# Kernel optimization log

Hardware: AMD Instinct MI355X
Metric: run time of the kernel (lower is better)

Reference implementation:

```python
import jax, jax.numpy as jnp
import numpy as np

N_GRAPHS = 32
N_NODES = 2048          # nodes per graph == lstm1 input_size
N_TOTAL = N_GRAPHS * N_NODES
N_EDGES = 1048576
HEADS = 8
GAT_OUT = 12            # per-head GAT output dim (== num_features)
OUT_CH = 9
NEG_SLOPE = 0.2
BN_EPS = 1e-5


def setup_inputs() -> dict:
    key = jax.random.key(0)
    ks = jax.random.split(key, 20)
    inp = {}
    inp['x'] = jax.random.normal(ks[0], (N_TOTAL, GAT_OUT), jnp.float32)
    inp['edge_index'] = jax.random.randint(ks[1], (2, N_EDGES), 0, N_TOTAL, jnp.int64)
    inp['W_gat'] = jax.random.normal(ks[2], (GAT_OUT, HEADS * GAT_OUT), jnp.float32) * 0.3
    inp['a_src'] = jax.random.normal(ks[3], (HEADS, GAT_OUT), jnp.float32) * 0.3
    inp['a_dst'] = jax.random.normal(ks[4], (HEADS, GAT_OUT), jnp.float32) * 0.3
    inp['gat_bias'] = jax.random.normal(ks[5], (GAT_OUT,), jnp.float32) * 0.1
    inp['bn_gamma'] = jax.random.uniform(ks[6], (GAT_OUT,), jnp.float32, 0.5, 1.5)
    inp['bn_beta'] = jax.random.normal(ks[7], (GAT_OUT,), jnp.float32) * 0.1
    inp['bn_mean'] = jax.random.normal(ks[8], (GAT_OUT,), jnp.float32) * 0.1
    inp['bn_var'] = jax.random.uniform(ks[9], (GAT_OUT,), jnp.float32, 0.5, 1.5)
    inp['w_ih1'] = jax.random.normal(ks[10], (4 * 32, N_NODES), jnp.float32) / np.sqrt(N_NODES)
    inp['w_hh1'] = jax.random.normal(ks[11], (4 * 32, 32), jnp.float32) / np.sqrt(32)
    inp['b_ih1'] = jnp.zeros((4 * 32,), jnp.float32)
    inp['b_hh1'] = jnp.zeros((4 * 32,), jnp.float32)
    inp['w_ih2'] = jax.random.normal(ks[12], (4 * 128, 32), jnp.float32) / np.sqrt(32)
    inp['w_hh2'] = jax.random.normal(ks[13], (4 * 128, 128), jnp.float32) / np.sqrt(128)
    inp['b_ih2'] = jnp.zeros((4 * 128,), jnp.float32)
    inp['b_hh2'] = jnp.zeros((4 * 128,), jnp.float32)
    inp['lin_w'] = jax.random.normal(ks[14], (N_NODES, 128), jnp.float32) / np.sqrt(128)
    inp['lin_b'] = jax.random.normal(ks[15], (N_NODES,), jnp.float32) * 0.1
    return inp


def _gat(x, edge_index, W, a_src, a_dst, bias):
    # PyG GATConv, heads=HEADS, out=GAT_OUT, concat=False (mean over heads), eval mode.
    N = x.shape[0]
    xp = (x @ W).reshape(N, HEADS, GAT_OUT)               # [N,H,C]
    loops = jnp.arange(N, dtype=edge_index.dtype)
    src = jnp.concatenate([edge_index[0], loops])
    dst = jnp.concatenate([edge_index[1], loops])
    asrc = jnp.einsum('nhc,hc->nh', xp, a_src)            # [N,H]
    adst = jnp.einsum('nhc,hc->nh', xp, a_dst)
    e = jax.nn.leaky_relu(asrc[src] + adst[dst], NEG_SLOPE)  # [E,H]
    m = jax.ops.segment_max(e, dst, num_segments=N)
    e = jnp.exp(e - m[dst])
    denom = jax.ops.segment_sum(e, dst, num_segments=N)
    alpha = e / (denom[dst] + 1e-16)
    msg = xp[src] * alpha[:, :, None]                     # [E,H,C]
    out = jax.ops.segment_sum(msg, dst, num_segments=N)   # [N,H,C]
    return out.mean(axis=1) + bias                        # concat=False -> head mean


def _lstm(x_seq, w_ih, w_hh, b_ih, b_hh):
    # x_seq: [T,B,I]; PyTorch gate order i,f,g,o.
    Hh = w_hh.shape[1]
    B = x_seq.shape[1]
    bias = b_ih + b_hh

    def step(carry, xt):
        h, c = carry
        gates = xt @ w_ih.T + h @ w_hh.T + bias
        i, f, g, o = jnp.split(gates, 4, axis=-1)
        c = jax.nn.sigmoid(f) * c + jax.nn.sigmoid(i) * jnp.tanh(g)
        h = jax.nn.sigmoid(o) * jnp.tanh(c)
        return (h, c), h

    init = (jnp.zeros((B, Hh), x_seq.dtype), jnp.zeros((B, Hh), x_seq.dtype))
    _, hs = jax.lax.scan(step, init, x_seq)
    return hs


def reference(x, edge_index, W_gat, a_src, a_dst, gat_bias,
              bn_gamma, bn_beta, bn_mean, bn_var,
              w_ih1, w_hh1, b_ih1, b_hh1,
              w_ih2, w_hh2, b_ih2, b_hh2,
              lin_w, lin_b):
    h = _gat(x, edge_index, W_gat, a_src, a_dst, gat_bias)          # [N,12]
    h = (h - bn_mean) / jnp.sqrt(bn_var + BN_EPS) * bn_gamma + bn_beta
    # dropout inactive in eval mode
    h = jax.nn.log_softmax(h, axis=1)
    h = h.reshape(N_GRAPHS, N_NODES, GAT_OUT)
    h = jnp.moveaxis(h, 2, 0)                                       # [T=12,B,n]
    h = _lstm(h, w_ih1, w_hh1, b_ih1, b_hh1)                        # [12,B,32]
    h = _lstm(h, w_ih2, w_hh2, b_ih2, b_hh2)                        # [12,B,128]
    h = h @ lin_w.T + lin_b                                         # [12,B,n]
    h = h[-OUT_CH:]                                                 # [9,B,n]
    h = jnp.moveaxis(h, 0, 2)                                       # [B,n,9]
    return h.reshape(N_GRAPHS * N_NODES, OUT_CH)
```

## Files before the change

kernel.cpp:

```cpp
#include <hip/hip_runtime.h>
#include <math.h>

#define N_EDGES_C 1048576
#define N_TOTAL_C 65536

typedef _Float16 h2v __attribute__((ext_vector_type(2)));
typedef int i4v __attribute__((ext_vector_type(4)));

#if defined(__has_builtin)
#if __has_builtin(__builtin_amdgcn_fdot2)
#define HAS_FDOT2 1
#endif
#endif

__device__ __forceinline__ float fdot2(h2v a, h2v b, float c) {
#ifdef HAS_FDOT2
    return __builtin_amdgcn_fdot2(a, b, c, false);
#else
    return c + (float)a.x * (float)b.x + (float)a.y * (float)b.y;
#endif
}

__device__ __forceinline__ float sigf(float x){ return 1.0f/(1.0f+expf(-x)); }
__device__ __forceinline__ float lrelu(float x){ return (x>=0.f)? x : 0.2f*x; }


__global__ void prep_kernel(const float* __restrict__ x, const float* __restrict__ Wg,
                            const float* __restrict__ a_src, const float* __restrict__ a_dst,
                            _Float16* __restrict__ xpp)
{
    int tid = threadIdx.x;
    __shared__ float Ws[12*96];
    __shared__ float as_s[96], ad_s[96];
    for (int i = tid; i < 1152; i += 256) Ws[i] = Wg[i];
    if (tid < 96) { as_s[tid] = a_src[tid]; ad_s[tid] = a_dst[tid]; }
    __syncthreads();
    int gid = blockIdx.x * 256 + tid;
    int n = gid >> 3;
    int h = gid & 7;
    const float4* xv = (const float4*)(x + (size_t)n * 12);
    float4 v0 = xv[0], v1 = xv[1], v2 = xv[2];
    float xr[12] = {v0.x,v0.y,v0.z,v0.w, v1.x,v1.y,v1.z,v1.w, v2.x,v2.y,v2.z,v2.w};
    float xp_[12];
    #pragma unroll
    for (int c = 0; c < 12; c++) {
        float acc = 0.f;
        #pragma unroll
        for (int k = 0; k < 12; k++) acc += xr[k] * Ws[k*96 + h*12 + c];
        xp_[c] = acc;
    }
    float sa = 0.f, sd = 0.f;
    #pragma unroll
    for (int c = 0; c < 12; c++) { sa += xp_[c]*as_s[h*12+c]; sd += xp_[c]*ad_s[h*12+c]; }
    union { _Float16 hh[16]; float ff[8]; float4 f4[2]; } s;
    #pragma unroll
    for (int c = 0; c < 12; c++) s.hh[c] = (_Float16)xp_[c];
    s.ff[6] = sa;
    s.ff[7] = sd;
    float4* o = (float4*)(xpp + (size_t)gid * 16);
    o[0] = s.f4[0];
    o[1] = s.f4[1];
}

__global__ __launch_bounds__(256)
void edge_hist(const int* __restrict__ ei, unsigned* __restrict__ cnt,
               unsigned* __restrict__ rank8)
{
    __shared__ unsigned hist[16384];
    int tid = threadIdx.x;
    int slice = blockIdx.x;
    for (int i = tid; i < 16384; i += 256) hist[i] = 0;
    __syncthreads();
    const i4v* dst4 = (const i4v*)(ei + N_EDGES_C) + slice*2048;
    for (int i = tid; i < 2048; i += 256) {
        i4v d = __builtin_nontemporal_load(&dst4[i]);
        int dd[4] = {d.x, d.y, d.z, d.w};
        unsigned packed = 0;
        #pragma unroll
        for (int j = 0; j < 4; j++) {
            int dj = dd[j];
            unsigned sh = (unsigned)(dj & 3) << 3;
            unsigned old = atomicAdd(&hist[dj >> 2], 1u << sh);
            packed |= ((old >> sh) & 0xffu) << (j*8);
        }
        __builtin_nontemporal_store(packed, &rank8[slice*2048 + i]);
    }
    __syncthreads();
    unsigned* cg = cnt + (size_t)slice*16384;
    for (int i = tid; i < 16384; i += 256) cg[i] = hist[i];
}

__global__ void slice_prefix(unsigned* __restrict__ cnt, int* __restrict__ deg)
{
    int w = blockIdx.x*256 + threadIdx.x;
    unsigned run = 0;
    unsigned* base = cnt + w;
    for (int s = 0; s < 128; s++) {
        unsigned v = base[(size_t)s*16384];
        base[(size_t)s*16384] = run;
        run += v;
    }
    ((int4*)deg)[w] = make_int4((int)(run & 255u), (int)((run >> 8) & 255u),
                                (int)((run >> 16) & 255u), (int)(run >> 24));
}

__global__ void scan_build(const int* __restrict__ deg, int* __restrict__ rowptr)
{
    __shared__ int sums[1024];
    int tid = threadIdx.x;
    int4 v[16];
    const int4* deg4 = (const int4*)deg;
    #pragma unroll
    for (int j = 0; j < 16; j++) v[j] = deg4[tid*16 + j];
    int s = 0;
    #pragma unroll
    for (int j = 0; j < 16; j++) s += v[j].x + v[j].y + v[j].z + v[j].w;
    sums[tid] = s;
    __syncthreads();
    for (int off = 1; off < 1024; off <<= 1) {
        int t = 0;
        if (tid >= off) t = sums[tid - off];
        __syncthreads();
        if (tid >= off) sums[tid] += t;
        __syncthreads();
    }
    int run = sums[tid] - s;
    int4* rp4 = (int4*)rowptr;
    #pragma unroll
    for (int j = 0; j < 16; j++) {
        int4 r;
        r.x = run; run += v[j].x;
        r.y = run; run += v[j].y;
        r.z = run; run += v[j].z;
        r.w = run; run += v[j].w;
        rp4[tid*16 + j] = r;
    }
    if (tid == 1023) rowptr[65536] = run;
}

__global__ void edge_scatter(const int* __restrict__ ei, const unsigned* __restrict__ rank8,
                             const unsigned* __restrict__ cnt, const int* __restrict__ rowptr,
                             int* __restrict__ csr)
{
    int g8 = blockIdx.x & 7;
    int slice = (blockIdx.x >> 3) & 127;
    int half = blockIdx.x >> 10;
    int base = slice*2048 + half*1024;
    const i4v* dst4 = (const i4v*)(ei + N_EDGES_C);
    const i4v* src4 = (const i4v*)ei;
    const unsigned* cslice = cnt + (size_t)slice*16384;
    for (int i = threadIdx.x; i < 1024; i += 256) {
        int idx = base + i;
        i4v d = __builtin_nontemporal_load(&dst4[idx]);
        i4v s = __builtin_nontemporal_load(&src4[idx]);
        unsigned r = __builtin_nontemporal_load(&rank8[idx]);
        int dd[4] = {d.x, d.y, d.z, d.w};
        int ss[4] = {s.x, s.y, s.z, s.w};
        #pragma unroll
        for (int j = 0; j < 4; j++) {
            int dj = dd[j];
            if ((dj >> 13) == g8) {
                unsigned word = cslice[dj >> 2];
                int so = (int)((word >> ((unsigned)(dj & 3) << 3)) & 0xffu);
                int rk = (int)((r >> (j*8)) & 0xffu);
                csr[rowptr[dj] + so + rk] = ss[j];
            }
        }
    }
}

__global__ void gat_aggregate(const _Float16* __restrict__ xpp,
                              const int* __restrict__ rowptr, const int* __restrict__ csr_src,
                              const float* __restrict__ gat_bias, const float* __restrict__ bn_gamma,
                              const float* __restrict__ bn_beta, const float* __restrict__ bn_mean,
                              const float* __restrict__ bn_var, float* __restrict__ seq)
{
    int gid = blockIdx.x * 256 + threadIdx.x;
    int n = gid >> 3;
    int h = gid & 7;

    float acc[12];
    float adst_n, d;
    {
        const float4* p = (const float4*)(xpp + (size_t)n*128 + h*16);
        float4 f0 = p[0], f1 = p[1];
        adst_n = f1.w;
        float w = __expf(lrelu(f1.z + adst_n));
        d = w;
        h2v c0 = __builtin_bit_cast(h2v, f0.x), c1 = __builtin_bit_cast(h2v, f0.y);
        h2v c2 = __builtin_bit_cast(h2v, f0.z), c3 = __builtin_bit_cast(h2v, f0.w);
        h2v c4 = __builtin_bit_cast(h2v, f1.x), c5 = __builtin_bit_cast(h2v, f1.y);
        acc[0]=w*(float)c0.x; acc[1]=w*(float)c0.y; acc[2]=w*(float)c1.x; acc[3]=w*(float)c1.y;
        acc[4]=w*(float)c2.x; acc[5]=w*(float)c2.y; acc[6]=w*(float)c3.x; acc[7]=w*(float)c3.y;
        acc[8]=w*(float)c4.x; acc[9]=w*(float)c4.y; acc[10]=w*(float)c5.x; acc[11]=w*(float)c5.y;
    }
    int beg = rowptr[n], end = rowptr[n+1];
    for (int i = beg; i < end; i++) {
        int src = csr_src[i];
        const float4* p = (const float4*)(xpp + (size_t)src*128 + h*16);
        float4 f0 = p[0], f1 = p[1];
        float w = __expf(lrelu(f1.z + adst_n));
        d += w;
        h2v c0 = __builtin_bit_cast(h2v, f0.x), c1 = __builtin_bit_cast(h2v, f0.y);
        h2v c2 = __builtin_bit_cast(h2v, f0.z), c3 = __builtin_bit_cast(h2v, f0.w);
        h2v c4 = __builtin_bit_cast(h2v, f1.x), c5 = __builtin_bit_cast(h2v, f1.y);
        acc[0]+=w*(float)c0.x; acc[1]+=w*(float)c0.y; acc[2]+=w*(float)c1.x; acc[3]+=w*(float)c1.y;
        acc[4]+=w*(float)c2.x; acc[5]+=w*(float)c2.y; acc[6]+=w*(float)c3.x; acc[7]+=w*(float)c3.y;
        acc[8]+=w*(float)c4.x; acc[9]+=w*(float)c4.y; acc[10]+=w*(float)c5.x; acc[11]+=w*(float)c5.y;
    }
    float inv = 1.0f / (d + 1e-16f);
    float res[12];
    #pragma unroll
    for (int c = 0; c < 12; c++) {
        float v = acc[c] * inv;
        v += __shfl_xor(v, 1);
        v += __shfl_xor(v, 2);
        v += __shfl_xor(v, 4);
        res[c] = v * 0.125f;
    }
    if (h == 0) {
        float vals[12];
        float mx = -1e30f;
        #pragma unroll
        for (int c = 0; c < 12; c++) {
            float v = res[c] + gat_bias[c];
            v = (v - bn_mean[c]) * rsqrtf(bn_var[c] + 1e-5f) * bn_gamma[c] + bn_beta[c];
            vals[c] = v;
            mx = fmaxf(mx, v);
        }
        float sum = 0.f;
        #pragma unroll
        for (int c = 0; c < 12; c++) sum += __expf(vals[c] - mx);
        float lse = __logf(sum) + mx;
        #pragma unroll
        for (int c = 0; c < 12; c++) seq[(size_t)c * N_TOTAL_C + n] = vals[c] - lse;
    }
}

__global__ void gemm_x1(const float* __restrict__ A, const float* __restrict__ B,
                        float* __restrict__ C)
{
    __shared__ float As[32][33], Bs[32][33];
    const int K = 2048, N = 128;
    int tid = threadIdx.x;
    int tx = tid & 31, ty = tid >> 5;
    int bm = blockIdx.x * 32, bn = blockIdx.y * 32;
    int kbase = blockIdx.z * 128;
    float acc[4] = {0.f,0.f,0.f,0.f};
    for (int kk = 0; kk < 128; kk += 32) {
        int k0 = kbase + kk;
        #pragma unroll
        for (int i = 0; i < 4; i++) {
            int r = ty + i*8;
            As[r][tx] = A[(size_t)(bm + r) * K + k0 + tx];
            Bs[r][tx] = B[(size_t)(bn + r) * K + k0 + tx];
        }
        __syncthreads();
        #pragma unroll
        for (int k = 0; k < 32; k++) {
            float bv = Bs[tx][k];
            #pragma unroll
            for (int i = 0; i < 4; i++) acc[i] += As[ty + i*8][k] * bv;
        }
        __syncthreads();
    }
    #pragma unroll
    for (int i = 0; i < 4; i++)
        atomicAdd(&C[(size_t)(bm + ty + i*8) * N + bn + tx], acc[i]);
}

__global__ __launch_bounds__(512)
void lstm_fused(const float* __restrict__ X1, const float* __restrict__ w_hh1,
                const float* __restrict__ b_ih1, const float* __restrict__ b_hh1,
                const float* __restrict__ w_ih2, const float* __restrict__ w_hh2,
                const float* __restrict__ b_ih2, const float* __restrict__ b_hh2,
                float* __restrict__ H2)
{
    __shared__ float whh1[128*33];
    __shared__ float b1s[128];
    __shared__ float h1[32], c1[32];
    __shared__ __align__(16) _Float16 h1s[32];
    __shared__ __align__(16) _Float16 h2s[128];
    __shared__ float c2[128];
    __shared__ float g1s[128], g2s[512];
    int tid = threadIdx.x;
    int b = blockIdx.x;

    h2v whh[64];
    {
        const float2* wh = (const float2*)(w_hh2 + (size_t)tid * 128);
        #pragma unroll
        for (int k = 0; k < 64; k++) {
            float2 v = wh[k];
            h2v t; t.x = (_Float16)v.x; t.y = (_Float16)v.y;
            whh[k] = t;
        }
    }
    h2v wih[16];
    {
        const float2* wi = (const float2*)(w_ih2 + (size_t)tid * 32);
        #pragma unroll
        for (int k = 0; k < 16; k++) {
            float2 v = wi[k];
            h2v t; t.x = (_Float16)v.x; t.y = (_Float16)v.y;
            wih[k] = t;
        }
    }
    float b2 = b_ih2[tid] + b_hh2[tid];

    for (int i = tid; i < 128*32; i += 512) whh1[(i >> 5)*33 + (i & 31)] = w_hh1[i];
    if (tid < 128) b1s[tid] = b_ih1[tid] + b_hh1[tid];
    if (tid < 32)  { h1[tid] = 0.f; c1[tid] = 0.f; h1s[tid] = (_Float16)0.f; }
    if (tid < 128) { c2[tid] = 0.f; h2s[tid] = (_Float16)0.f; }
    __syncthreads();

    for (int t = 0; t < 12; t++) {
        float p0 = b2, p1 = 0.f, p2 = 0.f, p3 = 0.f;
        #pragma unroll
        for (int j = 0; j < 16; j++) {
            float4 f = ((const float4*)h2s)[j];
            p0 = fdot2(__builtin_bit_cast(h2v, f.x), whh[j*4+0], p0);
            p1 = fdot2(__builtin_bit_cast(h2v, f.y), whh[j*4+1], p1);
            p2 = fdot2(__builtin_bit_cast(h2v, f.z), whh[j*4+2], p2);
            p3 = fdot2(__builtin_bit_cast(h2v, f.w), whh[j*4+3], p3);
        }
        float acc2 = (p0 + p1) + (p2 + p3);

        if (tid < 128) {
            const float* wr = &whh1[tid * 33];
            float acc = X1[((size_t)t*32 + b)*128 + tid] + b1s[tid];
            #pragma unroll
            for (int k = 0; k < 32; k++) acc += h1[k] * wr[k];
            g1s[tid] = acc;
        }
        __syncthreads();
        if (tid < 32) {
            float ig = sigf(g1s[tid]), fg = sigf(g1s[32+tid]);
            float gg = tanhf(g1s[64+tid]), og = sigf(g1s[96+tid]);
            float cn = fg * c1[tid] + ig * gg;
            c1[tid] = cn;
            float hn = og * tanhf(cn);
            h1[tid] = hn;
            h1s[tid] = (_Float16)hn;
        }
        __syncthreads();
        {
            float q0 = 0.f, q1 = 0.f, q2 = 0.f, q3 = 0.f;
            #pragma unroll
            for (int j = 0; j < 4; j++) {
                float4 f = ((const float4*)h1s)[j];
                q0 = fdot2(__builtin_bit_cast(h2v, f.x), wih[j*4+0], q0);
                q1 = fdot2(__builtin_bit_cast(h2v, f.y), wih[j*4+1], q1);
                q2 = fdot2(__builtin_bit_cast(h2v, f.z), wih[j*4+2], q2);
                q3 = fdot2(__builtin_bit_cast(h2v, f.w), wih[j*4+3], q3);
            }
            g2s[tid] = acc2 + (q0 + q1) + (q2 + q3);
        }
        __syncthreads();
        if (tid < 128) {
            float ig = sigf(g2s[tid]), fg = sigf(g2s[128+tid]);
            float gg = tanhf(g2s[256+tid]), og = sigf(g2s[384+tid]);
            float cn = fg * c2[tid] + ig * gg;
            c2[tid] = cn;
            float hn = og * tanhf(cn);
            h2s[tid] = (_Float16)hn;
            if (t >= 3) H2[((size_t)t*32 + b)*128 + tid] = hn;
        }
        __syncthreads();
    }
}

__global__ void gemm_out(const float* __restrict__ A, const float* __restrict__ B,
                         const float* __restrict__ bias, float* __restrict__ out)
{
    __shared__ float As[32][33], Bs[32][33];
    const int K = 128;
    int tid = threadIdx.x;
    int tx = tid & 31, ty = tid >> 5;
    int bm = blockIdx.x * 32, bn = blockIdx.y * 32;
    float acc[4] = {0.f,0.f,0.f,0.f};
    for (int k0 = 0; k0 < K; k0 += 32) {
        #pragma unroll
        for (int i = 0; i < 4; i++) {
            int r = ty + i*8;
            As[r][tx] = A[(size_t)(bm + r) * K + k0 + tx];
            Bs[r][tx] = B[(size_t)(bn + r) * K + k0 + tx];
        }
        __syncthreads();
        #pragma unroll
        for (int kk = 0; kk < 32; kk++) {
            float bv = Bs[tx][kk];
            #pragma unroll
            for (int i = 0; i < 4; i++) acc[i] += As[ty + i*8][kk] * bv;
        }
        __syncthreads();
    }
    int j = blockIdx.x;
    int nn = bn + tx;
    float bv = bias[nn];
    #pragma unroll
    for (int i = 0; i < 4; i++) {
        int bb = ty + i*8;
        out[((size_t)bb * 2048 + nn) * 9 + j] = acc[i] + bv;
    }
}

extern "C" void kernel_launch(void* const* d_in, const int* in_sizes, int n_in,
                              void* d_out, int out_size, void* d_ws, size_t ws_size,
                              hipStream_t stream)
{
    const float* x        = (const float*)d_in[0];
    const int*   ei       = (const int*)  d_in[1];
    const float* W_gat    = (const float*)d_in[2];
    const float* a_src    = (const float*)d_in[3];
    const float* a_dst    = (const float*)d_in[4];
    const float* gat_bias = (const float*)d_in[5];
    const float* bn_gamma = (const float*)d_in[6];
    const float* bn_beta  = (const float*)d_in[7];
    const float* bn_mean  = (const float*)d_in[8];
    const float* bn_var   = (const float*)d_in[9];
    const float* w_ih1    = (const float*)d_in[10];
    const float* w_hh1    = (const float*)d_in[11];
    const float* b_ih1    = (const float*)d_in[12];
    const float* b_hh1    = (const float*)d_in[13];
    const float* w_ih2    = (const float*)d_in[14];
    const float* w_hh2    = (const float*)d_in[15];
    const float* b_ih2    = (const float*)d_in[16];
    const float* b_hh2    = (const float*)d_in[17];
    const float* lin_w    = (const float*)d_in[18];
    const float* lin_b    = (const float*)d_in[19];
    float* out = (float*)d_out;

    float* ws = (float*)d_ws;
    _Float16* xpp = (_Float16*)ws;
    float* seq  = ws + 4194304;
    float* X1   = seq + 786432;
    float* H2   = X1  + 49152;
    int* rowptr = (int*)(H2 + 49152);
    int* deg    = rowptr + 65544;
    unsigned* cnt = (unsigned*)(deg + 65536);
    unsigned* rank8 = cnt + 2097152;
    int* csr    = (int*)(rank8 + 262144);

    hipMemsetAsync(X1, 0, 49152 * sizeof(float), stream);
    prep_kernel <<<2048, 256, 0, stream>>>(x, W_gat, a_src, a_dst, xpp);
    edge_hist   <<<128, 256, 0, stream>>>(ei, cnt, rank8);
    slice_prefix<<<64, 256, 0, stream>>>(cnt, deg);
    scan_build  <<<1, 1024, 0, stream>>>(deg, rowptr);
    edge_scatter<<<2048, 256, 0, stream>>>(ei, rank8, cnt, rowptr, csr);
    gat_aggregate<<<2048, 256, 0, stream>>>(xpp, rowptr, csr,
                                            gat_bias, bn_gamma, bn_beta, bn_mean, bn_var, seq);
    gemm_x1<<<dim3(12, 4, 16), 256, 0, stream>>>(seq, w_ih1, X1);
    lstm_fused<<<32, 512, 0, stream>>>(X1, w_hh1, b_ih1, b_hh1, w_ih2, w_hh2, b_ih2, b_hh2, H2);
    gemm_out<<<dim3(9, 64), 256, 0, stream>>>(H2 + 96*128, lin_w, lin_b, out);
}
```

Measured before the change: 270.7 us.

## Split GAT aggregation per head with head-major layout and separate combine kernel

```diff
diff --git a/kernel.cpp b/kernel.cpp
--- a/kernel.cpp
+++ b/kernel.cpp
@@ -27,9 +27,10 @@
 
 __global__ void prep_kernel(const float* __restrict__ x, const float* __restrict__ Wg,
                             const float* __restrict__ a_src, const float* __restrict__ a_dst,
-                            _Float16* __restrict__ xpp)
-{
-    int tid = threadIdx.x;
+                            _Float16* __restrict__ xph, float* __restrict__ X1)
+{
+    int tid = threadIdx.x;
+    if (blockIdx.x < 192) X1[blockIdx.x*256 + tid] = 0.f;
     __shared__ float Ws[12*96];
     __shared__ float as_s[96], ad_s[96];
     for (int i = tid; i < 1152; i += 256) Ws[i] = Wg[i];
@@ -57,7 +58,7 @@
     for (int c = 0; c < 12; c++) s.hh[c] = (_Float16)xp_[c];
     s.ff[6] = sa;
     s.ff[7] = sd;
-    float4* o = (float4*)(xpp + (size_t)gid * 16);
+    float4* o = (float4*)(xph + ((size_t)h*65536 + n)*16);
     o[0] = s.f4[0];
     o[1] = s.f4[1];
 }
@@ -169,72 +170,77 @@
     }
 }
 
-__global__ void gat_aggregate(const _Float16* __restrict__ xpp,
+__global__ void gat_aggregate(const _Float16* __restrict__ xph,
                               const int* __restrict__ rowptr, const int* __restrict__ csr_src,
-                              const float* __restrict__ gat_bias, const float* __restrict__ bn_gamma,
-                              const float* __restrict__ bn_beta, const float* __restrict__ bn_mean,
-                              const float* __restrict__ bn_var, float* __restrict__ seq)
-{
-    int gid = blockIdx.x * 256 + threadIdx.x;
-    int n = gid >> 3;
-    int h = gid & 7;
-
-    float acc[12];
-    float adst_n, d;
-    {
-        const float4* p = (const float4*)(xpp + (size_t)n*128 + h*16);
-        float4 f0 = p[0], f1 = p[1];
-        adst_n = f1.w;
-        float w = __expf(lrelu(f1.z + adst_n));
-        d = w;
-        h2v c0 = __builtin_bit_cast(h2v, f0.x), c1 = __builtin_bit_cast(h2v, f0.y);
-        h2v c2 = __builtin_bit_cast(h2v, f0.z), c3 = __builtin_bit_cast(h2v, f0.w);
-        h2v c4 = __builtin_bit_cast(h2v, f1.x), c5 = __builtin_bit_cast(h2v, f1.y);
-        acc[0]=w*(float)c0.x; acc[1]=w*(float)c0.y; acc[2]=w*(float)c1.x; acc[3]=w*(float)c1.y;
-        acc[4]=w*(float)c2.x; acc[5]=w*(float)c2.y; acc[6]=w*(float)c3.x; acc[7]=w*(float)c3.y;
-        acc[8]=w*(float)c4.x; acc[9]=w*(float)c4.y; acc[10]=w*(float)c5.x; acc[11]=w*(float)c5.y;
-    }
+                              _Float16* __restrict__ outh)
+{
+    int h = blockIdx.x & 7;
+    int chunk = blockIdx.x >> 3;
+    int tid = threadIdx.x;
+    int lane8 = tid & 7;
+    int n = chunk*32 + (tid >> 3);
+    const float* rowbase = (const float*)xph + (size_t)h*65536*8;
+    float fs = rowbase[(size_t)n*8 + lane8];
+    float adst_n = __shfl(fs, 7, 8);
+    float asrc_n = __shfl(fs, 6, 8);
+    float w = __expf(lrelu(asrc_n + adst_n));
+    float d = w;
+    h2v cs = __builtin_bit_cast(h2v, fs);
+    float a0 = w*(float)cs.x, a1 = w*(float)cs.y;
     int beg = rowptr[n], end = rowptr[n+1];
     for (int i = beg; i < end; i++) {
         int src = csr_src[i];
-        const float4* p = (const float4*)(xpp + (size_t)src*128 + h*16);
-        float4 f0 = p[0], f1 = p[1];
-        float w = __expf(lrelu(f1.z + adst_n));
-        d += w;
-        h2v c0 = __builtin_bit_cast(h2v, f0.x), c1 = __builtin_bit_cast(h2v, f0.y);
-        h2v c2 = __builtin_bit_cast(h2v, f0.z), c3 = __builtin_bit_cast(h2v, f0.w);
-        h2v c4 = __builtin_bit_cast(h2v, f1.x), c5 = __builtin_bit_cast(h2v, f1.y);
-        acc[0]+=w*(float)c0.x; acc[1]+=w*(float)c0.y; acc[2]+=w*(float)c1.x; acc[3]+=w*(float)c1.y;
-        acc[4]+=w*(float)c2.x; acc[5]+=w*(float)c2.y; acc[6]+=w*(float)c3.x; acc[7]+=w*(float)c3.y;
-        acc[8]+=w*(float)c4.x; acc[9]+=w*(float)c4.y; acc[10]+=w*(float)c5.x; acc[11]+=w*(float)c5.y;
-    }
-    float inv = 1.0f / (d + 1e-16f);
-    float res[12];
+        float f = rowbase[(size_t)src*8 + lane8];
+        float as = __shfl(f, 6, 8);
+        float wj = __expf(lrelu(as + adst_n));
+        d += wj;
+        h2v c = __builtin_bit_cast(h2v, f);
+        a0 += wj*(float)c.x;
+        a1 += wj*(float)c.y;
+    }
+    float inv = 0.125f / (d + 1e-16f);
+    if (lane8 < 6) {
+        h2v o;
+        o.x = (_Float16)(a0*inv);
+        o.y = (_Float16)(a1*inv);
+        *(h2v*)(outh + ((size_t)h*65536 + n)*12 + lane8*2) = o;
+    }
+}
+
+__global__ void combine_kernel(const _Float16* __restrict__ outh,
+                               const float* __restrict__ gat_bias, const float* __restrict__ bn_gamma,
+                               const float* __restrict__ bn_beta, const float* __restrict__ bn_mean,
+                               const float* __restrict__ bn_var, float* __restrict__ seq)
+{
+    int n = blockIdx.x*256 + threadIdx.x;
+    float v[12];
+    #pragma unroll
+    for (int c = 0; c < 12; c++) v[c] = 0.f;
+    #pragma unroll
+    for (int hh = 0; hh < 8; hh++) {
+        const h2v* p = (const h2v*)(outh + ((size_t)hh*65536 + n)*12);
+        #pragma unroll
+        for (int j = 0; j < 6; j++) {
+            h2v t = p[j];
+            v[j*2]   += (float)t.x;
+            v[j*2+1] += (float)t.y;
+        }
+    }
+    float vals[12];
+    float mx = -1e30f;
     #pragma unroll
     for (int c = 0; c < 12; c++) {
-        float v = acc[c] * inv;
-        v += __shfl_xor(v, 1);
-        v += __shfl_xor(v, 2);
-        v += __shfl_xor(v, 4);
-        res[c] = v * 0.125f;
-    }
-    if (h == 0) {
-        float vals[12];
-        float mx = -1e30f;
-        #pragma unroll
-        for (int c = 0; c < 12; c++) {
-            float v = res[c] + gat_bias[c];
-            v = (v - bn_mean[c]) * rsqrtf(bn_var[c] + 1e-5f) * bn_gamma[c] + bn_beta[c];
-            vals[c] = v;
-            mx = fmaxf(mx, v);
-        }
-        float sum = 0.f;
-        #pragma unroll
-        for (int c = 0; c < 12; c++) sum += __expf(vals[c] - mx);
-        float lse = __logf(sum) + mx;
-        #pragma unroll
-        for (int c = 0; c < 12; c++) seq[(size_t)c * N_TOTAL_C + n] = vals[c] - lse;
-    }
+        float t = v[c] + gat_bias[c];
+        t = (t - bn_mean[c]) * rsqrtf(bn_var[c] + 1e-5f) * bn_gamma[c] + bn_beta[c];
+        vals[c] = t;
+        mx = fmaxf(mx, t);
+    }
+    float sum = 0.f;
+    #pragma unroll
+    for (int c = 0; c < 12; c++) sum += __expf(vals[c] - mx);
+    float lse = __logf(sum) + mx;
+    #pragma unroll
+    for (int c = 0; c < 12; c++) seq[(size_t)c * N_TOTAL_C + n] = vals[c] - lse;
 }
 
 __global__ void gemm_x1(const float* __restrict__ A, const float* __restrict__ B,
@@ -432,24 +438,24 @@
     float* out = (float*)d_out;
 
     float* ws = (float*)d_ws;
-    _Float16* xpp = (_Float16*)ws;
+    _Float16* xph = (_Float16*)ws;
     float* seq  = ws + 4194304;
     float* X1   = seq + 786432;
     float* H2   = X1  + 49152;
     int* rowptr = (int*)(H2 + 49152);
     int* deg    = rowptr + 65544;
-    unsigned* cnt = (unsigned*)(deg + 65536);
+    int* csr    = deg + 65536;
+    unsigned* cnt = (unsigned*)(csr + 1048576);
     unsigned* rank8 = cnt + 2097152;
-    int* csr    = (int*)(rank8 + 262144);
-
-    hipMemsetAsync(X1, 0, 49152 * sizeof(float), stream);
-    prep_kernel <<<2048, 256, 0, stream>>>(x, W_gat, a_src, a_dst, xpp);
+    _Float16* outh = (_Float16*)cnt;
+
+    prep_kernel <<<2048, 256, 0, stream>>>(x, W_gat, a_src, a_dst, xph, X1);
     edge_hist   <<<128, 256, 0, stream>>>(ei, cnt, rank8);
     slice_prefix<<<64, 256, 0, stream>>>(cnt, deg);
     scan_build  <<<1, 1024, 0, stream>>>(deg, rowptr);
     edge_scatter<<<2048, 256, 0, stream>>>(ei, rank8, cnt, rowptr, csr);
-    gat_aggregate<<<2048, 256, 0, stream>>>(xpp, rowptr, csr,
-                                            gat_bias, bn_gamma, bn_beta, bn_mean, bn_var, seq);
+    gat_aggregate<<<16384, 256, 0, stream>>>(xph, rowptr, csr, outh);
+    combine_kernel<<<256, 256, 0, stream>>>(outh, gat_bias, bn_gamma, bn_beta, bn_mean, bn_var, seq);
     gemm_x1<<<dim3(12, 4, 16), 256, 0, stream>>>(seq, w_ih1, X1);
     lstm_fused<<<32, 512, 0, stream>>>(X1, w_hh1, b_ih1, b_hh1, w_ih2, w_hh2, b_ih2, b_hh2, H2);
     gemm_out<<<dim3(9, 64), 256, 0, stream>>>(H2 + 96*128, lin_w, lin_b, out);
```

Result: slower. 311.0 us (+14.9%).
